# Kernel optimization log

Hardware: AMD Instinct MI355X
Metric: run time of the kernel (lower is better)

## Reference

```python
import jax, jax.numpy as jnp
import numpy as np

D_MODEL = 512
N_HEADS = 8
D_K = D_MODEL // N_HEADS  # 64
WINDOW = 10               # hardcoded in Inter_Patch_Attention
CLAMP = 10000.0


def setup_inputs() -> dict:
    key = jax.random.key(0)
    ks = jax.random.split(key, 9)
    B, L = 4, 2048
    s_in = 1.0 / np.sqrt(D_MODEL)
    s_out = 1.0 / np.sqrt(N_HEADS * D_K)
    return {
        "Q": jax.random.normal(ks[0], (B, L, D_MODEL), jnp.float32),
        # Linear weights stored as [in, out]
        "Wq": jax.random.uniform(ks[1], (D_MODEL, N_HEADS * D_K), jnp.float32, -s_in, s_in),
        "bq": jax.random.uniform(ks[2], (N_HEADS * D_K,), jnp.float32, -s_in, s_in),
        "Wk": jax.random.uniform(ks[3], (D_MODEL, N_HEADS * D_K), jnp.float32, -s_in, s_in),
        "bk": jax.random.uniform(ks[4], (N_HEADS * D_K,), jnp.float32, -s_in, s_in),
        "Wv": jax.random.uniform(ks[5], (D_MODEL, N_HEADS * D_K), jnp.float32, -s_in, s_in),
        "bv": jax.random.uniform(ks[6], (N_HEADS * D_K,), jnp.float32, -s_in, s_in),
        "Wo": jax.random.uniform(ks[7], (N_HEADS * D_K, D_MODEL), jnp.float32, -s_out, s_out),
        "bo": jax.random.uniform(ks[8], (D_MODEL,), jnp.float32, -s_out, s_out),
    }


def _band_mask(q_len, k_len):
    # 0 inside the sliding window |i-j| <= WINDOW, -inf outside.
    # (rows with i >= k_len would be fully 0, but here q_len == k_len)
    i = jnp.arange(q_len)[:, None]
    j = jnp.arange(k_len)[None, :]
    inside = jnp.abs(i - j) <= WINDOW
    return jnp.where(inside, 0.0, -jnp.inf).astype(jnp.float32)


def reference(Q, Wq, bq, Wk, bk, Wv, bv, Wo, bo):
    B, L, _ = Q.shape
    scale = jnp.float32(D_K ** -0.5)  # nn.Parameter, non-trainable (lsa=False)

    # QKV projections -> [B, H, L, Dk]
    q = (Q @ Wq + bq).reshape(B, L, N_HEADS, D_K).transpose(0, 2, 1, 3)
    k = (Q @ Wk + bk).reshape(B, L, N_HEADS, D_K).transpose(0, 2, 1, 3)
    v = (Q @ Wv + bv).reshape(B, L, N_HEADS, D_K).transpose(0, 2, 1, 3)

    scores = jnp.einsum("bhqd,bhkd->bhqk", q, k) * scale
    scores = jnp.clip(scores, -CLAMP, CLAMP)
    scores = scores + _band_mask(L, L)[None, None]

    attn = jax.nn.softmax(scores, axis=-1)
    attn = jnp.nan_to_num(attn, nan=0.0, posinf=CLAMP, neginf=-CLAMP)

    out = jnp.einsum("bhqk,bhkd->bhqd", attn, v)
    out = jnp.nan_to_num(out, nan=0.0, posinf=CLAMP, neginf=-CLAMP)

    out = out.transpose(0, 2, 1, 3).reshape(B, L, N_HEADS * D_K)
    out = out @ Wo + bo
    return out
```

## Files before the change

### kernel.cpp

```cpp
#include <hip/hip_runtime.h>
#include <hip/hip_bf16.h>

typedef unsigned short u16;
typedef short bf16x8 __attribute__((ext_vector_type(8)));
typedef u16 u16x8 __attribute__((ext_vector_type(8)));
typedef u16 u16x4 __attribute__((ext_vector_type(4)));
typedef float f32x4 __attribute__((ext_vector_type(4)));

#define D_MODEL 512
#define L_SEQ 2048
#define B_SZ 4
#define N_HEADS 8
#define D_K 64
#define M_ROWS 8192
#define NQKV 1536
#define WIN 10

__device__ inline u16 f2bf(float x) {
  __hip_bfloat16 h = __float2bfloat16(x);
  return *reinterpret_cast<u16*>(&h);
}
__device__ inline float bf2f(u16 u) {
  __hip_bfloat16 h;
  *reinterpret_cast<u16*>(&h) = u;
  return __bfloat162float(h);
}

__device__ inline void stage16(const void* gptr, void* ldsptr) {
  void* g = const_cast<void*>(gptr);
  __builtin_amdgcn_global_load_lds(
      (__attribute__((address_space(1))) void*)g,
      (__attribute__((address_space(3))) void*)ldsptr, 16, 0, 0);
}

__global__ __launch_bounds__(256) void prep(
    const float* __restrict__ X, const float* __restrict__ Wq,
    const float* __restrict__ Wk, const float* __restrict__ Wv,
    const float* __restrict__ Wo, const float* __restrict__ bq,
    const float* __restrict__ bk, const float* __restrict__ bv,
    u16* __restrict__ Xh, u16* __restrict__ Bqkv, u16* __restrict__ Bo,
    float* __restrict__ bias_qkv) {
  __shared__ float wlds[64 * 65];
  int blk = blockIdx.x, t = threadIdx.x;
  if (blk < 4096) {
    int i = blk * 256 + t;
    float4 x = ((const float4*)X)[i];
    u16x4 o;
    o[0] = f2bf(x.x); o[1] = f2bf(x.y); o[2] = f2bf(x.z); o[3] = f2bf(x.w);
    *(u16x4*)(Xh + i * 4) = o;
    return;
  }
  if (blk < 4352) {
    int tid = blk - 4096;
    int which = tid >> 6;
    int t64 = tid & 63;
    int k0 = (t64 >> 3) * 64, n0 = (t64 & 7) * 64;
    const float* W = which == 0 ? Wq : which == 1 ? Wk : which == 2 ? Wv : Wo;
    int c = t & 63, g = t >> 6;
#pragma unroll
    for (int rr = 0; rr < 16; ++rr) {
      int kl = g * 16 + rr;
      wlds[kl * 65 + c] = W[(size_t)(k0 + kl) * 512 + n0 + c];
    }
    __syncthreads();
    u16* dst = which < 3 ? Bqkv : Bo;
    int nbase = which < 3 ? which * 512 : 0;
#pragma unroll
    for (int rr = 0; rr < 16; ++rr) {
      int nl = g * 16 + rr;
      float v = wlds[c * 65 + nl];
      dst[(size_t)(nbase + n0 + nl) * 512 + k0 + c] = f2bf(v);
    }
    return;
  }
  for (int i = t; i < 1536; i += 256)
    bias_qkv[i] = i < 512 ? bq[i] : i < 1024 ? bk[i - 512] : bv[i - 1024];
}

__global__ __launch_bounds__(256) void gemm_qkv(
    const u16* __restrict__ A, const u16* __restrict__ B,
    const float* __restrict__ bias, u16* __restrict__ C) {
  __shared__ u16 sA[2][128 * 32], sB[2][128 * 32];
  int t = threadIdx.x, w = t >> 6, lane = t & 63;
  int bid = blockIdx.y * 12 + blockIdx.x;
  int swz = (bid & 7) * 96 + (bid >> 3);
  long m0 = (long)(swz / 12) * 128, n0 = (long)(swz % 12) * 128;
  int wm = (w >> 1) * 64, wn = (w & 1) * 64;
  int fr = lane & 15, fo = lane >> 4;
  int rl = lane >> 2, cb = (lane & 3) * 16;
  const char* Ab = (const char*)A;
  const char* Bb = (const char*)B;

  f32x4 acc[4][4] = {};

#define STAGE_QKV(buf, kt)                                                  \
  do {                                                                      \
    int c0 = w, c1 = w + 4;                                                 \
    int r0 = c0 * 16 + rl, r1 = c1 * 16 + rl;                               \
    stage16(Ab + ((m0 + r0) * 512 + (long)(kt) * 32) * 2 + cb,              \
            (char*)sA[buf] + c0 * 1024);                                    \
    stage16(Bb + ((n0 + r0) * 512 + (long)(kt) * 32) * 2 + cb,              \
            (char*)sB[buf] + c0 * 1024);                                    \
    stage16(Ab + ((m0 + r1) * 512 + (long)(kt) * 32) * 2 + cb,              \
            (char*)sA[buf] + c1 * 1024);                                    \
    stage16(Bb + ((n0 + r1) * 512 + (long)(kt) * 32) * 2 + cb,              \
            (char*)sB[buf] + c1 * 1024);                                    \
  } while (0)

  STAGE_QKV(0, 0);
  __syncthreads();

  for (int kt = 0; kt < 16; ++kt) {
    int cur = kt & 1;
    if (kt < 15) STAGE_QKV(cur ^ 1, kt + 1);
    bf16x8 af[4], bf[4];
#pragma unroll
    for (int m = 0; m < 4; ++m)
      af[m] = *(const bf16x8*)&sA[cur][(wm + m * 16 + fr) * 32 + fo * 8];
#pragma unroll
    for (int n = 0; n < 4; ++n)
      bf[n] = *(const bf16x8*)&sB[cur][(wn + n * 16 + fr) * 32 + fo * 8];
#pragma unroll
    for (int m = 0; m < 4; ++m)
#pragma unroll
      for (int n = 0; n < 4; ++n)
        acc[m][n] = __builtin_amdgcn_mfma_f32_16x16x32_bf16(af[m], bf[n], acc[m][n], 0, 0, 0);
    __syncthreads();
  }
#undef STAGE_QKV

  int rbase = m0 + wm + fo * 4, cbase = n0 + wn + fr;
#pragma unroll
  for (int n = 0; n < 4; ++n) {
    int col = cbase + n * 16;
    float bn = bias[col];
#pragma unroll
    for (int m = 0; m < 4; ++m) {
      int row = rbase + m * 16;
#pragma unroll
      for (int q = 0; q < 4; ++q)
        C[(size_t)(row + q) * NQKV + col] = f2bf(acc[m][n][q] + bn);
    }
  }
}

__global__ __launch_bounds__(256) void gemm_o(
    const u16* __restrict__ A, const u16* __restrict__ B,
    const float* __restrict__ bias, float* __restrict__ C) {
  __shared__ u16 sA[2][64 * 32], sB[2][128 * 32];
  int t = threadIdx.x, w = t >> 6, lane = t & 63;
  int bid = blockIdx.y * 4 + blockIdx.x;
  int swz = (bid & 7) * 64 + (bid >> 3);
  long m0 = (long)(swz / 4) * 64, n0 = (long)(swz % 4) * 128;
  int wn = w * 32;
  int fr = lane & 15, fo = lane >> 4;
  int rl = lane >> 2, cb = (lane & 3) * 16;
  const char* Ab = (const char*)A;
  const char* Bb = (const char*)B;

  f32x4 acc[4][2] = {};

#define STAGE_O(buf, kt)                                                    \
  do {                                                                      \
    int ra = w * 16 + rl;                                                   \
    stage16(Ab + ((m0 + ra) * 512 + (long)(kt) * 32) * 2 + cb,              \
            (char*)sA[buf] + w * 1024);                                     \
    int c0 = w, c1 = w + 4;                                                 \
    int r0 = c0 * 16 + rl, r1 = c1 * 16 + rl;                               \
    stage16(Bb + ((n0 + r0) * 512 + (long)(kt) * 32) * 2 + cb,              \
            (char*)sB[buf] + c0 * 1024);                                    \
    stage16(Bb + ((n0 + r1) * 512 + (long)(kt) * 32) * 2 + cb,              \
            (char*)sB[buf] + c1 * 1024);                                    \
  } while (0)

  STAGE_O(0, 0);
  __syncthreads();

  for (int kt = 0; kt < 16; ++kt) {
    int cur = kt & 1;
    if (kt < 15) STAGE_O(cur ^ 1, kt + 1);
    bf16x8 af[4], bf[2];
#pragma unroll
    for (int m = 0; m < 4; ++m)
      af[m] = *(const bf16x8*)&sA[cur][(m * 16 + fr) * 32 + fo * 8];
#pragma unroll
    for (int n = 0; n < 2; ++n)
      bf[n] = *(const bf16x8*)&sB[cur][(wn + n * 16 + fr) * 32 + fo * 8];
#pragma unroll
    for (int m = 0; m < 4; ++m)
#pragma unroll
      for (int n = 0; n < 2; ++n)
        acc[m][n] = __builtin_amdgcn_mfma_f32_16x16x32_bf16(af[m], bf[n], acc[m][n], 0, 0, 0);
    __syncthreads();
  }
#undef STAGE_O

  int rbase = m0 + fo * 4, cbase = n0 + wn + fr;
#pragma unroll
  for (int n = 0; n < 2; ++n) {
    int col = cbase + n * 16;
    float bn = bias[col];
#pragma unroll
    for (int m = 0; m < 4; ++m) {
      int row = rbase + m * 16;
#pragma unroll
      for (int q = 0; q < 4; ++q)
        C[(size_t)(row + q) * 512 + col] = acc[m][n][q] + bn;
    }
  }
}

#define ATTN_LDS 73216

__global__ __launch_bounds__(256) void attn_mfma(const u16* __restrict__ QKV,
                                                 u16* __restrict__ AOh) {
  extern __shared__ char lds[];
  u16* sQ = (u16*)lds;
  u16* sK = (u16*)(lds + 18432);
  u16* sVT = (u16*)(lds + 41472);
  int t = threadIdx.x, w = t >> 6, lane = t & 63;
  u16* sP = (u16*)(lds + 64000 + w * 2304);

  int blk = blockIdx.x;
  int tile = blk & 15, h = (blk >> 4) & 7, b = blk >> 7;
  int l0 = tile * 128;
  const u16* base = QKV + (size_t)b * L_SEQ * NQKV + h * D_K;

#pragma unroll
  for (int i = 0; i < 4; ++i) {
    int task = t + i * 256;
    int row = task >> 3, oct = task & 7;
    u16x8 g = *(const u16x8*)(base + (size_t)(l0 + row) * NQKV + oct * 8);
    *(u16x8*)(sQ + row * 72 + oct * 8) = g;
  }
#pragma unroll
  for (int i = 0; i < 5; ++i) {
    int task = t + i * 256;
    int row = task >> 3, oct = task & 7;
    int l = min(max(l0 - 16 + row, 0), L_SEQ - 1);
    u16x8 g = *(const u16x8*)(base + (size_t)l * NQKV + 512 + oct * 8);
    *(u16x8*)(sK + row * 72 + oct * 8) = g;
  }
#pragma unroll
  for (int i = 0; i < 5; ++i) {
    int task = t + i * 256;
    int kv = task >> 3, oct = task & 7;
    int l = min(max(l0 - 16 + kv, 0), L_SEQ - 1);
    u16x8 g = *(const u16x8*)(base + (size_t)l * NQKV + 1024 + oct * 8);
#pragma unroll
    for (int e = 0; e < 8; ++e)
      sVT[(oct * 8 + e) * 176 + kv] = g[e];
  }
  if (t < 128) {
    u16x8 z = {};
    *(u16x8*)(sVT + (t >> 1) * 176 + 160 + (t & 1) * 8) = z;
  }
  if (lane < 32) {
    u16x8 z = {};
    *(u16x8*)(sP + (lane >> 1) * 72 + 48 + (lane & 1) * 8) = z;
  }
  __syncthreads();

  int fr = lane & 15, fo = lane >> 4;

  for (int qi = 0; qi < 2; ++qi) {
    if (qi) __syncthreads();
    int qt = w * 2 + qi;

    bf16x8 Aq[2];
#pragma unroll
    for (int ks = 0; ks < 2; ++ks)
      Aq[ks] = *(const bf16x8*)(sQ + (qt * 16 + fr) * 72 + ks * 32 + fo * 8);

    f32x4 sc[3] = {};
#pragma unroll
    for (int kt = 0; kt < 3; ++kt)
#pragma unroll
      for (int ks = 0; ks < 2; ++ks) {
        bf16x8 Bk = *(const bf16x8*)(sK + (qt * 16 + kt * 16 + fr) * 72 + ks * 32 + fo * 8);
        sc[kt] = __builtin_amdgcn_mfma_f32_16x16x32_bf16(Aq[ks], Bk, sc[kt], 0, 0, 0);
      }

    float pj[3][4], mj[4], rj[4];
#pragma unroll
    for (int j = 0; j < 4; ++j) {
      int irow = l0 + qt * 16 + fo * 4 + j;
      float mloc = -1.0e30f;
#pragma unroll
      for (int kt = 0; kt < 3; ++kt) {
        int jcol = l0 - 16 + qt * 16 + kt * 16 + fr;
        float sv = fminf(fmaxf(sc[kt][j] * 0.125f, -10000.f), 10000.f);
        int dd = irow - jcol;
        bool ok = (dd <= WIN) && (dd >= -WIN) && (jcol >= 0) && (jcol < L_SEQ);
        sv = ok ? sv : -1.0e30f;
        pj[kt][j] = sv;
        mloc = fmaxf(mloc, sv);
      }
      mj[j] = mloc;
    }
#pragma unroll
    for (int st = 1; st <= 8; st <<= 1)
#pragma unroll
      for (int j = 0; j < 4; ++j)
        mj[j] = fmaxf(mj[j], __shfl_xor(mj[j], st));
#pragma unroll
    for (int j = 0; j < 4; ++j) {
      float r = 0.f;
#pragma unroll
      for (int kt = 0; kt < 3; ++kt) {
        float e = (pj[kt][j] > -1.0e29f) ? __expf(pj[kt][j] - mj[j]) : 0.f;
        pj[kt][j] = e;
        r += e;
      }
      rj[j] = r;
    }
#pragma unroll
    for (int st = 1; st <= 8; st <<= 1)
#pragma unroll
      for (int j = 0; j < 4; ++j)
        rj[j] += __shfl_xor(rj[j], st);
#pragma unroll
    for (int j = 0; j < 4; ++j) rj[j] = 1.f / rj[j];

#pragma unroll
    for (int kt = 0; kt < 3; ++kt)
#pragma unroll
      for (int j = 0; j < 4; ++j)
        sP[(fo * 4 + j) * 72 + kt * 16 + fr] = f2bf(pj[kt][j] * rj[j]);

    f32x4 oa[4] = {};
#pragma unroll
    for (int ks = 0; ks < 2; ++ks) {
      bf16x8 Ap = *(const bf16x8*)(sP + fr * 72 + ks * 32 + fo * 8);
#pragma unroll
      for (int nt = 0; nt < 4; ++nt) {
        bf16x8 Bv = *(const bf16x8*)(sVT + (nt * 16 + fr) * 176 + qt * 16 + ks * 32 + fo * 8);
        oa[nt] = __builtin_amdgcn_mfma_f32_16x16x32_bf16(Ap, Bv, oa[nt], 0, 0, 0);
      }
    }

#pragma unroll
    for (int nt = 0; nt < 4; ++nt)
#pragma unroll
      for (int j = 0; j < 4; ++j) {
        size_t row = (size_t)b * L_SEQ + l0 + qt * 16 + fo * 4 + j;
        AOh[row * D_MODEL + h * D_K + nt * 16 + fr] = f2bf(oa[nt][j]);
      }
  }
}

extern "C" void kernel_launch(void* const* d_in, const int* in_sizes, int n_in,
                              void* d_out, int out_size, void* d_ws, size_t ws_size,
                              hipStream_t stream) {
  const float* Q  = (const float*)d_in[0];
  const float* Wq = (const float*)d_in[1];
  const float* bq = (const float*)d_in[2];
  const float* Wk = (const float*)d_in[3];
  const float* bk = (const float*)d_in[4];
  const float* Wv = (const float*)d_in[5];
  const float* bv = (const float*)d_in[6];
  const float* Wo = (const float*)d_in[7];
  const float* bo = (const float*)d_in[8];
  float* out = (float*)d_out;

  char* p = (char*)d_ws;
  u16* Xh = (u16*)p;        p += (size_t)M_ROWS * 512 * 2;
  u16* Bqkv = (u16*)p;      p += (size_t)1536 * 512 * 2;
  u16* Bo = (u16*)p;        p += (size_t)512 * 512 * 2;
  float* bias_qkv = (float*)p; p += 1536 * 4;
  u16* QKV = (u16*)p;       p += (size_t)M_ROWS * 1536 * 2;
  u16* AOh = (u16*)p;       p += (size_t)M_ROWS * 512 * 2;

  hipFuncSetAttribute((const void*)attn_mfma,
                      hipFuncAttributeMaxDynamicSharedMemorySize, ATTN_LDS);

  hipLaunchKernelGGL(prep, dim3(4353), dim3(256), 0, stream,
                     Q, Wq, Wk, Wv, Wo, bq, bk, bv, Xh, Bqkv, Bo, bias_qkv);

  gemm_qkv<<<dim3(12, 64), dim3(256), 0, stream>>>(Xh, Bqkv, bias_qkv, QKV);

  hipLaunchKernelGGL(attn_mfma, dim3(512), dim3(256), ATTN_LDS, stream, QKV, AOh);

  gemm_o<<<dim3(4, 128), dim3(256), 0, stream>>>(AOh, Bo, bo, out);
}
```

Measured before the change: 59.61 us.

## Fuse fp32-to-bf16 activation conversion into QKV GEMM A-tile loading

Removes the separate pass in prep that converted the input activations to bf16, and instead has gemm_qkv load fp32 X directly through registers, convert to bf16, and write into a padded LDS tile (row stride 40) that is double-buffered. This drops a full write and reread of the 8 MB-scale bf16 activation copy. In exchange each GEMM block rereads fp32 activations (twice the bytes) for every one of the 12 column tiles, and A is staged through registers instead of direct global-to-LDS loads, which adds VGPR pressure and VALU conversion work inside the main loop.

After: 63.72 us. +6.9%, slower.

```diff
diff --git a/kernel.cpp b/kernel.cpp
--- a/kernel.cpp
+++ b/kernel.cpp
@@ -34,26 +34,16 @@
 }
 
 __global__ __launch_bounds__(256) void prep(
-    const float* __restrict__ X, const float* __restrict__ Wq,
-    const float* __restrict__ Wk, const float* __restrict__ Wv,
-    const float* __restrict__ Wo, const float* __restrict__ bq,
-    const float* __restrict__ bk, const float* __restrict__ bv,
-    u16* __restrict__ Xh, u16* __restrict__ Bqkv, u16* __restrict__ Bo,
-    float* __restrict__ bias_qkv) {
+    const float* __restrict__ Wq, const float* __restrict__ Wk,
+    const float* __restrict__ Wv, const float* __restrict__ Wo,
+    const float* __restrict__ bq, const float* __restrict__ bk,
+    const float* __restrict__ bv,
+    u16* __restrict__ Bqkv, u16* __restrict__ Bo, float* __restrict__ bias_qkv) {
   __shared__ float wlds[64 * 65];
   int blk = blockIdx.x, t = threadIdx.x;
-  if (blk < 4096) {
-    int i = blk * 256 + t;
-    float4 x = ((const float4*)X)[i];
-    u16x4 o;
-    o[0] = f2bf(x.x); o[1] = f2bf(x.y); o[2] = f2bf(x.z); o[3] = f2bf(x.w);
-    *(u16x4*)(Xh + i * 4) = o;
-    return;
-  }
-  if (blk < 4352) {
-    int tid = blk - 4096;
-    int which = tid >> 6;
-    int t64 = tid & 63;
+  if (blk < 256) {
+    int which = blk >> 6;
+    int t64 = blk & 63;
     int k0 = (t64 >> 3) * 64, n0 = (t64 & 7) * 64;
     const float* W = which == 0 ? Wq : which == 1 ? Wk : which == 2 ? Wv : Wo;
     int c = t & 63, g = t >> 6;
@@ -77,10 +67,12 @@
     bias_qkv[i] = i < 512 ? bq[i] : i < 1024 ? bk[i - 512] : bv[i - 1024];
 }
 
+#define LDA40 40
+
 __global__ __launch_bounds__(256) void gemm_qkv(
-    const u16* __restrict__ A, const u16* __restrict__ B,
+    const float* __restrict__ X, const u16* __restrict__ B,
     const float* __restrict__ bias, u16* __restrict__ C) {
-  __shared__ u16 sA[2][128 * 32], sB[2][128 * 32];
+  __shared__ u16 sA[2][128 * LDA40], sB[2][128 * 32];
   int t = threadIdx.x, w = t >> 6, lane = t & 63;
   int bid = blockIdx.y * 12 + blockIdx.x;
   int swz = (bid & 7) * 96 + (bid >> 3);
@@ -88,35 +80,59 @@
   int wm = (w >> 1) * 64, wn = (w & 1) * 64;
   int fr = lane & 15, fo = lane >> 4;
   int rl = lane >> 2, cb = (lane & 3) * 16;
-  const char* Ab = (const char*)A;
   const char* Bb = (const char*)B;
 
+  int arow = t >> 1, ach = (t & 1) * 16;
+
   f32x4 acc[4][4] = {};
 
-#define STAGE_QKV(buf, kt)                                                  \
+#define STAGE_B(buf, kt)                                                    \
   do {                                                                      \
     int c0 = w, c1 = w + 4;                                                 \
     int r0 = c0 * 16 + rl, r1 = c1 * 16 + rl;                               \
-    stage16(Ab + ((m0 + r0) * 512 + (long)(kt) * 32) * 2 + cb,              \
-            (char*)sA[buf] + c0 * 1024);                                    \
     stage16(Bb + ((n0 + r0) * 512 + (long)(kt) * 32) * 2 + cb,              \
             (char*)sB[buf] + c0 * 1024);                                    \
-    stage16(Ab + ((m0 + r1) * 512 + (long)(kt) * 32) * 2 + cb,              \
-            (char*)sA[buf] + c1 * 1024);                                    \
     stage16(Bb + ((n0 + r1) * 512 + (long)(kt) * 32) * 2 + cb,              \
             (char*)sB[buf] + c1 * 1024);                                    \
   } while (0)
 
-  STAGE_QKV(0, 0);
+#define LOAD_A(kt)                                                          \
+  do {                                                                      \
+    const float* src = X + (m0 + arow) * 512 + (long)(kt) * 32 + ach;       \
+    av[0] = *(const float4*)(src);                                          \
+    av[1] = *(const float4*)(src + 4);                                      \
+    av[2] = *(const float4*)(src + 8);                                      \
+    av[3] = *(const float4*)(src + 12);                                     \
+  } while (0)
+
+#define WRITE_A(buf)                                                        \
+  do {                                                                      \
+    const float* fp = (const float*)av;                                     \
+    u16x8 w0, w1;                                                           \
+    _Pragma("unroll") for (int e = 0; e < 8; ++e) {                         \
+      w0[e] = f2bf(fp[e]);                                                  \
+      w1[e] = f2bf(fp[e + 8]);                                              \
+    }                                                                       \
+    *(u16x8*)&sA[buf][arow * LDA40 + ach] = w0;                             \
+    *(u16x8*)&sA[buf][arow * LDA40 + ach + 8] = w1;                         \
+  } while (0)
+
+  float4 av[4];
+  LOAD_A(0);
+  STAGE_B(0, 0);
+  WRITE_A(0);
   __syncthreads();
 
   for (int kt = 0; kt < 16; ++kt) {
     int cur = kt & 1;
-    if (kt < 15) STAGE_QKV(cur ^ 1, kt + 1);
+    if (kt < 15) {
+      LOAD_A(kt + 1);
+      STAGE_B(cur ^ 1, kt + 1);
+    }
     bf16x8 af[4], bf[4];
 #pragma unroll
     for (int m = 0; m < 4; ++m)
-      af[m] = *(const bf16x8*)&sA[cur][(wm + m * 16 + fr) * 32 + fo * 8];
+      af[m] = *(const bf16x8*)&sA[cur][(wm + m * 16 + fr) * LDA40 + fo * 8];
 #pragma unroll
     for (int n = 0; n < 4; ++n)
       bf[n] = *(const bf16x8*)&sB[cur][(wn + n * 16 + fr) * 32 + fo * 8];
@@ -125,9 +141,12 @@
 #pragma unroll
       for (int n = 0; n < 4; ++n)
         acc[m][n] = __builtin_amdgcn_mfma_f32_16x16x32_bf16(af[m], bf[n], acc[m][n], 0, 0, 0);
+    if (kt < 15) WRITE_A(cur ^ 1);
     __syncthreads();
   }
-#undef STAGE_QKV
+#undef STAGE_B
+#undef LOAD_A
+#undef WRITE_A
 
   int rbase = m0 + wm + fo * 4, cbase = n0 + wn + fr;
 #pragma unroll
@@ -364,7 +383,6 @@
   float* out = (float*)d_out;
 
   char* p = (char*)d_ws;
-  u16* Xh = (u16*)p;        p += (size_t)M_ROWS * 512 * 2;
   u16* Bqkv = (u16*)p;      p += (size_t)1536 * 512 * 2;
   u16* Bo = (u16*)p;        p += (size_t)512 * 512 * 2;
   float* bias_qkv = (float*)p; p += 1536 * 4;
@@ -374,10 +392,10 @@
   hipFuncSetAttribute((const void*)attn_mfma,
                       hipFuncAttributeMaxDynamicSharedMemorySize, ATTN_LDS);
 
-  hipLaunchKernelGGL(prep, dim3(4353), dim3(256), 0, stream,
-                     Q, Wq, Wk, Wv, Wo, bq, bk, bv, Xh, Bqkv, Bo, bias_qkv);
-
-  gemm_qkv<<<dim3(12, 64), dim3(256), 0, stream>>>(Xh, Bqkv, bias_qkv, QKV);
+  hipLaunchKernelGGL(prep, dim3(257), dim3(256), 0, stream,
+                     Wq, Wk, Wv, Wo, bq, bk, bv, Bqkv, Bo, bias_qkv);
+
+  gemm_qkv<<<dim3(12, 64), dim3(256), 0, stream>>>(Q, Bqkv, bias_qkv, QKV);
 
   hipLaunchKernelGGL(attn_mfma, dim3(512), dim3(256), ATTN_LDS, stream, QKV, AOh);
 
```

## Triple-buffer GEMM LDS staging with explicit vmcnt waits and single barrier

Applied to the files above, without the earlier changes.

Converts the QKV and output-projection GEMMs from double to triple buffering. Loads run two K-tiles ahead, and fine-grained s_waitcnt vmcnt waits plus one raw barrier per iteration replace the two __syncthreads. This lets global-to-LDS loads overlap more of the MFMA work and removes one barrier per step. In exchange it uses more LDS per block, which may lower occupancy, and it relies on hand-counted vmcnt values that must match the number of async loads issued per stage.

New measurement: 55.39 us. 1.08x faster.

```diff
diff --git a/kernel.cpp b/kernel.cpp
--- a/kernel.cpp
+++ b/kernel.cpp
@@ -32,6 +32,20 @@
       (__attribute__((address_space(1))) void*)g,
       (__attribute__((address_space(3))) void*)ldsptr, 16, 0, 0);
 }
+
+template <int N>
+__device__ inline void vmwait() {
+  asm volatile("s_waitcnt vmcnt(%0)" ::"i"(N) : "memory");
+}
+__device__ inline void lgkm0() {
+  asm volatile("s_waitcnt lgkmcnt(0)" ::: "memory");
+}
+#define BARX()                      \
+  do {                              \
+    asm volatile("" ::: "memory");  \
+    __builtin_amdgcn_s_barrier();   \
+    asm volatile("" ::: "memory");  \
+  } while (0)
 
 __global__ __launch_bounds__(256) void prep(
     const float* __restrict__ X, const float* __restrict__ Wq,
@@ -80,7 +94,7 @@
 __global__ __launch_bounds__(256) void gemm_qkv(
     const u16* __restrict__ A, const u16* __restrict__ B,
     const float* __restrict__ bias, u16* __restrict__ C) {
-  __shared__ u16 sA[2][128 * 32], sB[2][128 * 32];
+  __shared__ u16 sA[3][128 * 32], sB[3][128 * 32];
   int t = threadIdx.x, w = t >> 6, lane = t & 63;
   int bid = blockIdx.y * 12 + blockIdx.x;
   int swz = (bid & 7) * 96 + (bid >> 3);
@@ -108,11 +122,12 @@
   } while (0)
 
   STAGE_QKV(0, 0);
-  __syncthreads();
+  STAGE_QKV(1, 1);
 
   for (int kt = 0; kt < 16; ++kt) {
-    int cur = kt & 1;
-    if (kt < 15) STAGE_QKV(cur ^ 1, kt + 1);
+    int cur = kt % 3;
+    if (kt < 15) vmwait<4>(); else vmwait<0>();
+    BARX();
     bf16x8 af[4], bf[4];
 #pragma unroll
     for (int m = 0; m < 4; ++m)
@@ -120,12 +135,13 @@
 #pragma unroll
     for (int n = 0; n < 4; ++n)
       bf[n] = *(const bf16x8*)&sB[cur][(wn + n * 16 + fr) * 32 + fo * 8];
+    if (kt < 14) STAGE_QKV((kt + 2) % 3, kt + 2);
 #pragma unroll
     for (int m = 0; m < 4; ++m)
 #pragma unroll
       for (int n = 0; n < 4; ++n)
         acc[m][n] = __builtin_amdgcn_mfma_f32_16x16x32_bf16(af[m], bf[n], acc[m][n], 0, 0, 0);
-    __syncthreads();
+    lgkm0();
   }
 #undef STAGE_QKV
 
@@ -147,7 +163,7 @@
 __global__ __launch_bounds__(256) void gemm_o(
     const u16* __restrict__ A, const u16* __restrict__ B,
     const float* __restrict__ bias, float* __restrict__ C) {
-  __shared__ u16 sA[2][64 * 32], sB[2][128 * 32];
+  __shared__ u16 sA[3][64 * 32], sB[3][128 * 32];
   int t = threadIdx.x, w = t >> 6, lane = t & 63;
   int bid = blockIdx.y * 4 + blockIdx.x;
   int swz = (bid & 7) * 64 + (bid >> 3);
@@ -174,11 +190,12 @@
   } while (0)
 
   STAGE_O(0, 0);
-  __syncthreads();
+  STAGE_O(1, 1);
 
   for (int kt = 0; kt < 16; ++kt) {
-    int cur = kt & 1;
-    if (kt < 15) STAGE_O(cur ^ 1, kt + 1);
+    int cur = kt % 3;
+    if (kt < 15) vmwait<3>(); else vmwait<0>();
+    BARX();
     bf16x8 af[4], bf[2];
 #pragma unroll
     for (int m = 0; m < 4; ++m)
@@ -186,12 +203,13 @@
 #pragma unroll
     for (int n = 0; n < 2; ++n)
       bf[n] = *(const bf16x8*)&sB[cur][(wn + n * 16 + fr) * 32 + fo * 8];
+    if (kt < 14) STAGE_O((kt + 2) % 3, kt + 2);
 #pragma unroll
     for (int m = 0; m < 4; ++m)
 #pragma unroll
       for (int n = 0; n < 2; ++n)
         acc[m][n] = __builtin_amdgcn_mfma_f32_16x16x32_bf16(af[m], bf[n], acc[m][n], 0, 0, 0);
-    __syncthreads();
+    lgkm0();
   }
 #undef STAGE_O
 
```

## Load GEMM operands directly from global into registers, dropping LDS staging

Applied to the files above, without the earlier changes.

Both projection GEMMs (QKV and output) now read MFMA fragments straight from global memory into registers. A two-set register double buffer replaces the LDS double buffer filled with global_load_lds, which also removes the per-iteration barriers and the shared memory. The cost is that data shared across waves (each A row tile is used by two waves in gemm_qkv, and all four waves read the same A tile in gemm_o) is no longer loaded once per block into LDS. It now relies on L1/L2 hits, with more global load instructions and higher register pressure.

New measurement: 101.2 us. +69.8%, slower.

```diff
diff --git a/kernel.cpp b/kernel.cpp
--- a/kernel.cpp
+++ b/kernel.cpp
@@ -24,13 +24,6 @@
   __hip_bfloat16 h;
   *reinterpret_cast<u16*>(&h) = u;
   return __bfloat162float(h);
-}
-
-__device__ inline void stage16(const void* gptr, void* ldsptr) {
-  void* g = const_cast<void*>(gptr);
-  __builtin_amdgcn_global_load_lds(
-      (__attribute__((address_space(1))) void*)g,
-      (__attribute__((address_space(3))) void*)ldsptr, 16, 0, 0);
 }
 
 __global__ __launch_bounds__(256) void prep(
@@ -80,54 +73,45 @@
 __global__ __launch_bounds__(256) void gemm_qkv(
     const u16* __restrict__ A, const u16* __restrict__ B,
     const float* __restrict__ bias, u16* __restrict__ C) {
-  __shared__ u16 sA[2][128 * 32], sB[2][128 * 32];
   int t = threadIdx.x, w = t >> 6, lane = t & 63;
   int bid = blockIdx.y * 12 + blockIdx.x;
   int swz = (bid & 7) * 96 + (bid >> 3);
   long m0 = (long)(swz / 12) * 128, n0 = (long)(swz % 12) * 128;
   int wm = (w >> 1) * 64, wn = (w & 1) * 64;
   int fr = lane & 15, fo = lane >> 4;
-  int rl = lane >> 2, cb = (lane & 3) * 16;
-  const char* Ab = (const char*)A;
-  const char* Bb = (const char*)B;
+
+  const u16* Ap = A + (m0 + wm + fr) * 512 + fo * 8;
+  const u16* Bp = B + (n0 + wn + fr) * 512 + fo * 8;
 
   f32x4 acc[4][4] = {};
-
-#define STAGE_QKV(buf, kt)                                                  \
-  do {                                                                      \
-    int c0 = w, c1 = w + 4;                                                 \
-    int r0 = c0 * 16 + rl, r1 = c1 * 16 + rl;                               \
-    stage16(Ab + ((m0 + r0) * 512 + (long)(kt) * 32) * 2 + cb,              \
-            (char*)sA[buf] + c0 * 1024);                                    \
-    stage16(Bb + ((n0 + r0) * 512 + (long)(kt) * 32) * 2 + cb,              \
-            (char*)sB[buf] + c0 * 1024);                                    \
-    stage16(Ab + ((m0 + r1) * 512 + (long)(kt) * 32) * 2 + cb,              \
-            (char*)sA[buf] + c1 * 1024);                                    \
-    stage16(Bb + ((n0 + r1) * 512 + (long)(kt) * 32) * 2 + cb,              \
-            (char*)sB[buf] + c1 * 1024);                                    \
+  bf16x8 a0[4], b0[4], a1[4], b1[4];
+
+#define LOADSET(as, bs, kt)                                          \
+  do {                                                               \
+    _Pragma("unroll") for (int m = 0; m < 4; ++m)                    \
+        as[m] = *(const bf16x8*)(Ap + m * 16 * 512 + (kt) * 32);     \
+    _Pragma("unroll") for (int n = 0; n < 4; ++n)                    \
+        bs[n] = *(const bf16x8*)(Bp + n * 16 * 512 + (kt) * 32);     \
   } while (0)
 
-  STAGE_QKV(0, 0);
-  __syncthreads();
-
-  for (int kt = 0; kt < 16; ++kt) {
-    int cur = kt & 1;
-    if (kt < 15) STAGE_QKV(cur ^ 1, kt + 1);
-    bf16x8 af[4], bf[4];
-#pragma unroll
-    for (int m = 0; m < 4; ++m)
-      af[m] = *(const bf16x8*)&sA[cur][(wm + m * 16 + fr) * 32 + fo * 8];
-#pragma unroll
-    for (int n = 0; n < 4; ++n)
-      bf[n] = *(const bf16x8*)&sB[cur][(wn + n * 16 + fr) * 32 + fo * 8];
-#pragma unroll
-    for (int m = 0; m < 4; ++m)
-#pragma unroll
-      for (int n = 0; n < 4; ++n)
-        acc[m][n] = __builtin_amdgcn_mfma_f32_16x16x32_bf16(af[m], bf[n], acc[m][n], 0, 0, 0);
-    __syncthreads();
-  }
-#undef STAGE_QKV
+#define MFMASET(as, bs)                                              \
+  do {                                                               \
+    _Pragma("unroll") for (int m = 0; m < 4; ++m)                    \
+        _Pragma("unroll") for (int n = 0; n < 4; ++n)                \
+            acc[m][n] = __builtin_amdgcn_mfma_f32_16x16x32_bf16(     \
+                as[m], bs[n], acc[m][n], 0, 0, 0);                   \
+  } while (0)
+
+  LOADSET(a0, b0, 0);
+#pragma unroll
+  for (int kt = 0; kt < 16; kt += 2) {
+    if (kt + 1 < 16) LOADSET(a1, b1, kt + 1);
+    MFMASET(a0, b0);
+    if (kt + 2 < 16) LOADSET(a0, b0, kt + 2);
+    MFMASET(a1, b1);
+  }
+#undef LOADSET
+#undef MFMASET
 
   int rbase = m0 + wm + fo * 4, cbase = n0 + wn + fr;
 #pragma unroll
@@ -147,53 +131,45 @@
 __global__ __launch_bounds__(256) void gemm_o(
     const u16* __restrict__ A, const u16* __restrict__ B,
     const float* __restrict__ bias, float* __restrict__ C) {
-  __shared__ u16 sA[2][64 * 32], sB[2][128 * 32];
   int t = threadIdx.x, w = t >> 6, lane = t & 63;
   int bid = blockIdx.y * 4 + blockIdx.x;
   int swz = (bid & 7) * 64 + (bid >> 3);
   long m0 = (long)(swz / 4) * 64, n0 = (long)(swz % 4) * 128;
   int wn = w * 32;
   int fr = lane & 15, fo = lane >> 4;
-  int rl = lane >> 2, cb = (lane & 3) * 16;
-  const char* Ab = (const char*)A;
-  const char* Bb = (const char*)B;
+
+  const u16* Ap = A + (m0 + fr) * 512 + fo * 8;
+  const u16* Bp = B + (n0 + wn + fr) * 512 + fo * 8;
 
   f32x4 acc[4][2] = {};
-
-#define STAGE_O(buf, kt)                                                    \
-  do {                                                                      \
-    int ra = w * 16 + rl;                                                   \
-    stage16(Ab + ((m0 + ra) * 512 + (long)(kt) * 32) * 2 + cb,              \
-            (char*)sA[buf] + w * 1024);                                     \
-    int c0 = w, c1 = w + 4;                                                 \
-    int r0 = c0 * 16 + rl, r1 = c1 * 16 + rl;                               \
-    stage16(Bb + ((n0 + r0) * 512 + (long)(kt) * 32) * 2 + cb,              \
-            (char*)sB[buf] + c0 * 1024);                                    \
-    stage16(Bb + ((n0 + r1) * 512 + (long)(kt) * 32) * 2 + cb,              \
-            (char*)sB[buf] + c1 * 1024);                                    \
+  bf16x8 a0[4], b0[2], a1[4], b1[2];
+
+#define LOADSET(as, bs, kt)                                          \
+  do {                                                               \
+    _Pragma("unroll") for (int m = 0; m < 4; ++m)                    \
+        as[m] = *(const bf16x8*)(Ap + m * 16 * 512 + (kt) * 32);     \
+    _Pragma("unroll") for (int n = 0; n < 2; ++n)                    \
+        bs[n] = *(const bf16x8*)(Bp + n * 16 * 512 + (kt) * 32);     \
   } while (0)
 
-  STAGE_O(0, 0);
-  __syncthreads();
-
-  for (int kt = 0; kt < 16; ++kt) {
-    int cur = kt & 1;
-    if (kt < 15) STAGE_O(cur ^ 1, kt + 1);
-    bf16x8 af[4], bf[2];
-#pragma unroll
-    for (int m = 0; m < 4; ++m)
-      af[m] = *(const bf16x8*)&sA[cur][(m * 16 + fr) * 32 + fo * 8];
-#pragma unroll
-    for (int n = 0; n < 2; ++n)
-      bf[n] = *(const bf16x8*)&sB[cur][(wn + n * 16 + fr) * 32 + fo * 8];
-#pragma unroll
-    for (int m = 0; m < 4; ++m)
-#pragma unroll
-      for (int n = 0; n < 2; ++n)
-        acc[m][n] = __builtin_amdgcn_mfma_f32_16x16x32_bf16(af[m], bf[n], acc[m][n], 0, 0, 0);
-    __syncthreads();
-  }
-#undef STAGE_O
+#define MFMASET(as, bs)                                              \
+  do {                                                               \
+    _Pragma("unroll") for (int m = 0; m < 4; ++m)                    \
+        _Pragma("unroll") for (int n = 0; n < 2; ++n)                \
+            acc[m][n] = __builtin_amdgcn_mfma_f32_16x16x32_bf16(     \
+                as[m], bs[n], acc[m][n], 0, 0, 0);                   \
+  } while (0)
+
+  LOADSET(a0, b0, 0);
+#pragma unroll
+  for (int kt = 0; kt < 16; kt += 2) {
+    if (kt + 1 < 16) LOADSET(a1, b1, kt + 1);
+    MFMASET(a0, b0);
+    if (kt + 2 < 16) LOADSET(a0, b0, kt + 2);
+    MFMASET(a1, b1);
+  }
+#undef LOADSET
+#undef MFMASET
 
   int rbase = m0 + fo * 4, cbase = n0 + wn + fr;
 #pragma unroll
```
